# Kernel tuning notes

Measured on AMD Instinct MI355X. Metric: run time of the kernel, lower is better.

Reference implementation:

```python
import jax, jax.numpy as jnp
import numpy as np

CV_CHAN = 49  # displacement channels; radius = (CV_CHAN - 1) // 2 = 24


def conv1x1(x, W, b):
    # x: [B,C,H,Wd], W: [O,C], b: [O] -> [B,O,H,Wd]
    return jnp.einsum('oc,bchw->bohw', W, x) + b[None, :, None, None]


def corr_volume(f1, f2, radius, eps):
    """Shift-and-dot correlation along width. f1,f2: [B,C,H,W] -> [B,2r+1,H,W].
    Channel k corresponds to displacement d = k - radius; out-of-range positions are 0
    (handled by zero-padding, matching the torch zero-filled shifted tensors)."""
    f1n = f1 / (jnp.linalg.norm(f1, axis=1, keepdims=True) + eps)
    f2n = f2 / (jnp.linalg.norm(f2, axis=1, keepdims=True) + eps)
    Wd = f1.shape[3]
    pad = jnp.pad(f2n, ((0, 0), (0, 0), (0, 0), (radius, radius)))
    # shifted_k[x] = f2n[x - d] = pad[x + 2*radius - k]
    slices = [
        jnp.sum(f1n * jax.lax.dynamic_slice_in_dim(pad, 2 * radius - k, Wd, axis=3), axis=1)
        for k in range(2 * radius + 1)
    ]
    return jnp.stack(slices, axis=1)


def setup_inputs() -> dict:
    key = jax.random.key(0)
    ks = jax.random.split(key, 10)
    B, C, H, W = 4, 128, 128, 256
    F = 128  # fmap channels
    G = 96   # geo encoder output channels
    s = 0.05
    return {
        'feat_l1': jax.random.normal(ks[0], (B, C, H, W), jnp.float32),
        'feat_r1': jax.random.normal(ks[1], (B, C, H, W), jnp.float32),
        'cv0': jax.random.normal(ks[2], (B, CV_CHAN, H, W), jnp.float32),
        'cv1': jax.random.normal(ks[3], (B, CV_CHAN, H, W), jnp.float32),
        'cv2': jax.random.normal(ks[4], (B, CV_CHAN, H, W), jnp.float32),
        'W_f1': jax.random.normal(ks[5], (F, C), jnp.float32) * s,
        'b_f1': jnp.zeros((F,), jnp.float32),
        'W_f2': jax.random.normal(ks[6], (F, C), jnp.float32) * s,
        'b_f2': jnp.zeros((F,), jnp.float32),
        'W_geo': jax.random.normal(ks[7], (G, CV_CHAN), jnp.float32) * s,
        'b_geo': jnp.zeros((G,), jnp.float32),
        'W_sel': jax.random.normal(ks[8], (3, 3 * G), jnp.float32) * s,
        'b_sel': jnp.zeros((3,), jnp.float32),
    }


def reference(feat_l1, feat_r1, cv0, cv1, cv2,
              W_f1, b_f1, W_f2, b_f2, W_geo, b_geo, W_sel, b_sel):
    # init feature maps (init_fmap1 / init_fmap2 as 1x1 convs)
    fmap1 = conv1x1(feat_l1, W_f1, b_f1)
    fmap2 = conv1x1(feat_r1, W_f2, b_f2)
    radius = (CV_CHAN - 1) // 2
    init_corr = corr_volume(fmap1, fmap2, radius, 1e-8)  # [B, CV_CHAN, H, W]

    # geo_volume2 (1x1 conv CV_CHAN -> 96) applied to each geometric volume
    g0 = conv1x1(cv0, W_geo, b_geo)
    g1 = conv1x1(cv1, W_geo, b_geo)
    g2 = conv1x1(cv2, W_geo, b_geo)
    combined_g = jnp.concatenate([g0, g1, g2], axis=1)  # [B, 288, H, W]

    logits = conv1x1(combined_g, W_sel, b_sel)           # [B, 3, H, W]
    w = jax.nn.softmax(logits, axis=1)

    weighted = (w[:, 0:1] * cv0[:, :CV_CHAN]
                + w[:, 1:2] * cv1[:, :CV_CHAN]
                + w[:, 2:3] * cv2[:, :CV_CHAN])
    final = init_corr + weighted
    return (final, init_corr, w)
```

## Files before the change

kernel.cpp:

```cpp
#include <hip/hip_runtime.h>

#define HW 32768
#define WIDTH 256

typedef float f32x4 __attribute__((ext_vector_type(4)));
typedef short s16x8 __attribute__((ext_vector_type(8)));

__device__ __forceinline__ unsigned short f2bf(float f){
    unsigned int u = __float_as_uint(f);
    u += 0x7FFFu + ((u >> 16) & 1u);
    return (unsigned short)(u >> 16);
}
__device__ __forceinline__ unsigned int pk2(float a, float b){
    return (unsigned int)f2bf(a) | ((unsigned int)f2bf(b) << 16);
}

__global__ __launch_bounds__(256, 2) void k_fmap(
    const float* __restrict__ fl, const float* __restrict__ fr,
    const float* __restrict__ W1, const float* __restrict__ W2,
    const float* __restrict__ b1, const float* __restrict__ b2,
    unsigned short* __restrict__ f1N, unsigned short* __restrict__ f2N)
{
    const int z = blockIdx.z;
    const float* feat = z ? fr : fl;
    const float* Wm   = z ? W2 : W1;
    const float* bias = z ? b2 : b1;
    unsigned short* out = z ? f2N : f1N;

    const int b    = blockIdx.y;
    const int pxb  = blockIdx.x * 256;
    const int tid  = threadIdx.x;
    const int wv   = tid >> 6;
    const int lane = tid & 63;
    const int quad = lane >> 4;
    const int l15  = lane & 15;

    __shared__ unsigned short Xs[32][260];
    __shared__ unsigned short Ws[128][40];

    f32x4 acc[8][4];
    #pragma unroll
    for (int m = 0; m < 8; ++m)
        #pragma unroll
        for (int nt = 0; nt < 4; ++nt)
            acc[m][nt] = (f32x4){0.f,0.f,0.f,0.f};

    const float* featB = feat + (size_t)b * 128 * HW + pxb;

    for (int kk = 0; kk < 4; ++kk){
        const int kc0 = kk * 32;
        __syncthreads();
        #pragma unroll
        for (int i = 0; i < 8; ++i){
            int u   = tid + i * 256;
            int row = u >> 6;
            int cp  = (u & 63) << 2;
            f32x4 v = *(const f32x4*)(featB + (size_t)(kc0 + row) * HW + cp);
            uint2 pk; pk.x = pk2(v[0], v[1]); pk.y = pk2(v[2], v[3]);
            *(uint2*)&Xs[row][cp] = pk;
        }
        #pragma unroll
        for (int i = 0; i < 4; ++i){
            int u   = tid + i * 256;
            int row = u >> 3;
            int cp  = (u & 7) << 2;
            f32x4 v = *(const f32x4*)(Wm + row * 128 + kc0 + cp);
            uint2 pk; pk.x = pk2(v[0], v[1]); pk.y = pk2(v[2], v[3]);
            *(uint2*)&Ws[row][cp] = pk;
        }
        __syncthreads();

        s16x8 af[8];
        #pragma unroll
        for (int m = 0; m < 8; ++m)
            af[m] = *(const s16x8*)&Ws[m * 16 + l15][quad * 8];

        #pragma unroll
        for (int nt = 0; nt < 4; ++nt){
            const int px = wv * 64 + nt * 16 + l15;
            s16x8 bf;
            #pragma unroll
            for (int j = 0; j < 8; ++j)
                bf[j] = (short)Xs[quad * 8 + j][px];
            #pragma unroll
            for (int m = 0; m < 8; ++m)
                acc[m][nt] = __builtin_amdgcn_mfma_f32_16x16x32_bf16(af[m], bf, acc[m][nt], 0, 0, 0);
        }
    }

    #pragma unroll
    for (int nt = 0; nt < 4; ++nt){
        const int px = wv * 64 + nt * 16 + l15;
        #pragma unroll
        for (int m = 0; m < 8; ++m){
            f32x4 bv = *(const f32x4*)(bias + m * 16 + quad * 4);
            acc[m][nt] += bv;
        }
        float n2 = 0.f;
        #pragma unroll
        for (int m = 0; m < 8; ++m)
            #pragma unroll
            for (int r = 0; r < 4; ++r)
                n2 += acc[m][nt][r] * acc[m][nt][r];
        n2 += __shfl_xor(n2, 16, 64);
        n2 += __shfl_xor(n2, 32, 64);
        const float scale = 1.f / (sqrtf(n2) + 1e-8f);
        unsigned short* orow = out + ((size_t)b * HW + pxb + px) * 128;
        #pragma unroll
        for (int m = 0; m < 8; ++m){
            uint2 pk;
            pk.x = pk2(acc[m][nt][0] * scale, acc[m][nt][1] * scale);
            pk.y = pk2(acc[m][nt][2] * scale, acc[m][nt][3] * scale);
            *(uint2*)(orow + m * 16 + quad * 4) = pk;
        }
    }
}

__global__ __launch_bounds__(256, 4) void k_corr(
    const unsigned short* __restrict__ f1N,
    const unsigned short* __restrict__ f2N,
    float* __restrict__ ic)
{
    const int tid  = threadIdx.x;
    const int wv   = tid >> 6;
    const int lane = tid & 63;
    const int quad = lane >> 4;
    const int l15  = lane & 15;

    const int strip = blockIdx.x * 4 + wv;
    const int b   = strip >> 11;
    const int rem = strip & 2047;
    const int h   = rem >> 4;
    const int x0  = (rem & 15) << 4;

    const size_t rowbase = (size_t)b * HW + (size_t)h * WIDTH;

    const unsigned short* arow = f1N + (rowbase + x0 + l15) * 128;
    s16x8 af[4];
    #pragma unroll
    for (int kk = 0; kk < 4; ++kk)
        af[kk] = *(const s16x8*)(arow + kk * 32 + quad * 8);

    f32x4 acc[4];
    #pragma unroll
    for (int nt = 0; nt < 4; ++nt) acc[nt] = (f32x4){0.f,0.f,0.f,0.f};

    #pragma unroll
    for (int nt = 0; nt < 4; ++nt){
        const int s = x0 + nt * 16 + l15 - 24;
        const bool valid = (s >= 0) && (s < WIDTH);
        const unsigned short* brow = f2N + (rowbase + s) * 128;
        #pragma unroll
        for (int kk = 0; kk < 4; ++kk){
            s16x8 bf = (s16x8){0,0,0,0,0,0,0,0};
            if (valid) bf = *(const s16x8*)(brow + kk * 32 + quad * 8);
            acc[nt] = __builtin_amdgcn_mfma_f32_16x16x32_bf16(af[kk], bf, acc[nt], 0, 0, 0);
        }
    }

    __shared__ float G[4][16][68];
    #pragma unroll
    for (int nt = 0; nt < 4; ++nt)
        #pragma unroll
        for (int r = 0; r < 4; ++r)
            G[wv][quad * 4 + r][nt * 16 + l15] = acc[nt][r];
    __syncthreads();

    float* obase = ic + (size_t)b * 49 * HW + (size_t)h * WIDTH + x0;
    #pragma unroll
    for (int i = 0; i < 13; ++i){
        int dd = quad + i * 4;
        if (dd < 49){
            float v = G[wv][l15][l15 + 48 - dd];
            obase[(size_t)dd * HW + l15] = v;
        }
    }
}

__global__ void k_prep(const float* __restrict__ Wsel, const float* __restrict__ bsel,
                       const float* __restrict__ Wgeo, const float* __restrict__ bgeo,
                       float* __restrict__ M, float* __restrict__ c0)
{
    int u = threadIdx.x;
    if (u < 441){
        int s = u / 147; int r = u % 147; int i = r / 49; int k = r % 49;
        float acc = 0.f;
        for (int o = 0; o < 96; ++o)
            acc += Wsel[s * 288 + i * 96 + o] * Wgeo[o * 49 + k];
        M[u] = acc;
    } else if (u < 444){
        int s = u - 441;
        float acc = bsel[s];
        for (int i = 0; i < 3; ++i)
            for (int o = 0; o < 96; ++o)
                acc += Wsel[s * 288 + i * 96 + o] * bgeo[o];
        c0[s] = acc;
    }
}

__global__ __launch_bounds__(256, 4) void k_sel(
    const float* __restrict__ cv0, const float* __restrict__ cv1, const float* __restrict__ cv2,
    const float* __restrict__ M, const float* __restrict__ c0,
    const float* __restrict__ ic,
    float* __restrict__ finalO, float* __restrict__ wO)
{
    __shared__ float Ms[441];
    __shared__ float c0s[3];
    const int tid = threadIdx.x;
    for (int i = tid; i < 441; i += 256) Ms[i] = M[i];
    if (tid < 3) c0s[tid] = c0[tid];
    __syncthreads();

    const int gid = blockIdx.x * 256 + tid;
    const int b = gid >> 15;
    const int p = gid & 32767;
    const size_t base = (size_t)b * 49 * HW + p;

    float lg0 = c0s[0], lg1 = c0s[1], lg2 = c0s[2];
    for (int k = 0; k < 49; ++k){
        size_t o = base + (size_t)k * HW;
        float v0 = cv0[o], v1 = cv1[o], v2 = cv2[o];
        lg0 += Ms[k]       * v0 + Ms[49  + k] * v1 + Ms[98  + k] * v2;
        lg1 += Ms[147 + k] * v0 + Ms[196 + k] * v1 + Ms[245 + k] * v2;
        lg2 += Ms[294 + k] * v0 + Ms[343 + k] * v1 + Ms[392 + k] * v2;
    }
    float mx = fmaxf(lg0, fmaxf(lg1, lg2));
    float e0 = expf(lg0 - mx), e1 = expf(lg1 - mx), e2 = expf(lg2 - mx);
    float inv = 1.f / (e0 + e1 + e2);
    float w0 = e0 * inv, w1 = e1 * inv, w2 = e2 * inv;

    const size_t wbase = (size_t)b * 3 * HW + p;
    wO[wbase]          = w0;
    wO[wbase + HW]     = w1;
    wO[wbase + 2 * HW] = w2;

    for (int k = 0; k < 49; ++k){
        size_t o = base + (size_t)k * HW;
        finalO[o] = ic[o] + w0 * cv0[o] + w1 * cv1[o] + w2 * cv2[o];
    }
}

extern "C" void kernel_launch(void* const* d_in, const int* in_sizes, int n_in,
                              void* d_out, int out_size, void* d_ws, size_t ws_size,
                              hipStream_t stream)
{
    const float* feat_l1 = (const float*)d_in[0];
    const float* feat_r1 = (const float*)d_in[1];
    const float* cv0     = (const float*)d_in[2];
    const float* cv1     = (const float*)d_in[3];
    const float* cv2     = (const float*)d_in[4];
    const float* W_f1    = (const float*)d_in[5];
    const float* b_f1    = (const float*)d_in[6];
    const float* W_f2    = (const float*)d_in[7];
    const float* b_f2    = (const float*)d_in[8];
    const float* W_geo   = (const float*)d_in[9];
    const float* b_geo   = (const float*)d_in[10];
    const float* W_sel   = (const float*)d_in[11];
    const float* b_sel   = (const float*)d_in[12];

    float* finalO = (float*)d_out;
    float* icO    = (float*)d_out + 6422528;
    float* wO     = (float*)d_out + 12845056;

    unsigned short* f1N = (unsigned short*)d_ws;
    unsigned short* f2N = (unsigned short*)((char*)d_ws + 33554432);
    float* Mbuf  = (float*)((char*)d_ws + 67108864);
    float* c0buf = Mbuf + 441;

    k_prep<<<1, 512, 0, stream>>>(W_sel, b_sel, W_geo, b_geo, Mbuf, c0buf);
    k_fmap<<<dim3(128, 4, 2), 256, 0, stream>>>(feat_l1, feat_r1, W_f1, W_f2, b_f1, b_f2, f1N, f2N);
    k_corr<<<2048, 256, 0, stream>>>(f1N, f2N, icO);
    k_sel<<<512, 256, 0, stream>>>(cv0, cv1, cv2, Mbuf, c0buf, icO, finalO, wO);
}
```

Baseline: 307.0 us.

## Load fmap operands directly from global, stage output through LDS, cache cv values in registers

The fmap GEMM now reads weights and features straight from global memory into bf16 MFMA fragments instead of staging them in shared memory. The normalized output is transposed through a shared tile so each thread writes contiguous 16-byte chunks. The selection kernel keeps all 147 cv values per pixel in registers, so the second pass no longer re-reads cv0/1/2, and its occupancy hint is lowered to fit that register use. The risks are strided, uncoalesced feature loads in the GEMM and register pressure or spills in k_sel.

```diff
diff --git a/kernel.cpp b/kernel.cpp
--- a/kernel.cpp
+++ b/kernel.cpp
@@ -35,9 +35,6 @@
     const int quad = lane >> 4;
     const int l15  = lane & 15;
 
-    __shared__ unsigned short Xs[32][260];
-    __shared__ unsigned short Ws[128][40];
-
     f32x4 acc[8][4];
     #pragma unroll
     for (int m = 0; m < 8; ++m)
@@ -47,50 +44,44 @@
 
     const float* featB = feat + (size_t)b * 128 * HW + pxb;
 
+    #pragma unroll
     for (int kk = 0; kk < 4; ++kk){
         const int kc0 = kk * 32;
-        __syncthreads();
-        #pragma unroll
-        for (int i = 0; i < 8; ++i){
-            int u   = tid + i * 256;
-            int row = u >> 6;
-            int cp  = (u & 63) << 2;
-            f32x4 v = *(const f32x4*)(featB + (size_t)(kc0 + row) * HW + cp);
-            uint2 pk; pk.x = pk2(v[0], v[1]); pk.y = pk2(v[2], v[3]);
-            *(uint2*)&Xs[row][cp] = pk;
-        }
-        #pragma unroll
-        for (int i = 0; i < 4; ++i){
-            int u   = tid + i * 256;
-            int row = u >> 3;
-            int cp  = (u & 7) << 2;
-            f32x4 v = *(const f32x4*)(Wm + row * 128 + kc0 + cp);
-            uint2 pk; pk.x = pk2(v[0], v[1]); pk.y = pk2(v[2], v[3]);
-            *(uint2*)&Ws[row][cp] = pk;
-        }
-        __syncthreads();
 
         s16x8 af[8];
         #pragma unroll
-        for (int m = 0; m < 8; ++m)
-            af[m] = *(const s16x8*)&Ws[m * 16 + l15][quad * 8];
+        for (int m = 0; m < 8; ++m){
+            const float* wp = Wm + (m * 16 + l15) * 128 + kc0 + quad * 8;
+            f32x4 w0 = *(const f32x4*)wp;
+            f32x4 w1 = *(const f32x4*)(wp + 4);
+            union { unsigned int u[4]; s16x8 v; } r;
+            r.u[0] = pk2(w0[0], w0[1]); r.u[1] = pk2(w0[2], w0[3]);
+            r.u[2] = pk2(w1[0], w1[1]); r.u[3] = pk2(w1[2], w1[3]);
+            af[m] = r.v;
+        }
 
         #pragma unroll
         for (int nt = 0; nt < 4; ++nt){
             const int px = wv * 64 + nt * 16 + l15;
-            s16x8 bf;
+            const float* bp = featB + (size_t)(kc0 + quad * 8) * HW + px;
+            float x[8];
             #pragma unroll
             for (int j = 0; j < 8; ++j)
-                bf[j] = (short)Xs[quad * 8 + j][px];
+                x[j] = bp[(size_t)j * HW];
+            union { unsigned int u[4]; s16x8 v; } r;
+            r.u[0] = pk2(x[0], x[1]); r.u[1] = pk2(x[2], x[3]);
+            r.u[2] = pk2(x[4], x[5]); r.u[3] = pk2(x[6], x[7]);
+            const s16x8 bf = r.v;
             #pragma unroll
             for (int m = 0; m < 8; ++m)
                 acc[m][nt] = __builtin_amdgcn_mfma_f32_16x16x32_bf16(af[m], bf, acc[m][nt], 0, 0, 0);
         }
     }
 
-    #pragma unroll
+    __shared__ unsigned short Ts[64][132];
+
     for (int nt = 0; nt < 4; ++nt){
-        const int px = wv * 64 + nt * 16 + l15;
+        __syncthreads();
         #pragma unroll
         for (int m = 0; m < 8; ++m){
             f32x4 bv = *(const f32x4*)(bias + m * 16 + quad * 4);
@@ -105,13 +96,29 @@
         n2 += __shfl_xor(n2, 16, 64);
         n2 += __shfl_xor(n2, 32, 64);
         const float scale = 1.f / (sqrtf(n2) + 1e-8f);
-        unsigned short* orow = out + ((size_t)b * HW + pxb + px) * 128;
+
+        unsigned short* trow = &Ts[wv * 16 + l15][0];
         #pragma unroll
         for (int m = 0; m < 8; ++m){
             uint2 pk;
             pk.x = pk2(acc[m][nt][0] * scale, acc[m][nt][1] * scale);
             pk.y = pk2(acc[m][nt][2] * scale, acc[m][nt][3] * scale);
-            *(uint2*)(orow + m * 16 + quad * 4) = pk;
+            *(uint2*)(trow + m * 16 + quad * 4) = pk;
+        }
+        __syncthreads();
+
+        const int s  = tid >> 2;
+        const int ch = tid & 3;
+        const int wvs = s >> 4, ls = s & 15;
+        const int gpx = pxb + wvs * 64 + nt * 16 + ls;
+        const unsigned short* src = &Ts[s][ch * 32];
+        unsigned short* dst = out + ((size_t)b * HW + gpx) * 128 + ch * 32;
+        #pragma unroll
+        for (int i = 0; i < 4; ++i){
+            union { struct { uint2 a, c; } p; s16x8 v; } m;
+            m.p.a = *(const uint2*)(src + i * 8);
+            m.p.c = *(const uint2*)(src + i * 8 + 4);
+            *(s16x8*)(dst + i * 8) = m.v;
         }
     }
 }
@@ -198,7 +205,7 @@
     }
 }
 
-__global__ __launch_bounds__(256, 4) void k_sel(
+__global__ __launch_bounds__(256, 2) void k_sel(
     const float* __restrict__ cv0, const float* __restrict__ cv1, const float* __restrict__ cv2,
     const float* __restrict__ M, const float* __restrict__ c0,
     const float* __restrict__ ic,
@@ -216,13 +223,19 @@
     const int p = gid & 32767;
     const size_t base = (size_t)b * 49 * HW + p;
 
-    float lg0 = c0s[0], lg1 = c0s[1], lg2 = c0s[2];
+    float a0[49], a1[49], a2[49];
+    #pragma unroll
     for (int k = 0; k < 49; ++k){
         size_t o = base + (size_t)k * HW;
-        float v0 = cv0[o], v1 = cv1[o], v2 = cv2[o];
-        lg0 += Ms[k]       * v0 + Ms[49  + k] * v1 + Ms[98  + k] * v2;
-        lg1 += Ms[147 + k] * v0 + Ms[196 + k] * v1 + Ms[245 + k] * v2;
-        lg2 += Ms[294 + k] * v0 + Ms[343 + k] * v1 + Ms[392 + k] * v2;
+        a0[k] = cv0[o]; a1[k] = cv1[o]; a2[k] = cv2[o];
+    }
+
+    float lg0 = c0s[0], lg1 = c0s[1], lg2 = c0s[2];
+    #pragma unroll
+    for (int k = 0; k < 49; ++k){
+        lg0 += Ms[k]       * a0[k] + Ms[49  + k] * a1[k] + Ms[98  + k] * a2[k];
+        lg1 += Ms[147 + k] * a0[k] + Ms[196 + k] * a1[k] + Ms[245 + k] * a2[k];
+        lg2 += Ms[294 + k] * a0[k] + Ms[343 + k] * a1[k] + Ms[392 + k] * a2[k];
     }
     float mx = fmaxf(lg0, fmaxf(lg1, lg2));
     float e0 = expf(lg0 - mx), e1 = expf(lg1 - mx), e2 = expf(lg2 - mx);
@@ -234,9 +247,10 @@
     wO[wbase + HW]     = w1;
     wO[wbase + 2 * HW] = w2;
 
+    #pragma unroll
     for (int k = 0; k < 49; ++k){
         size_t o = base + (size_t)k * HW;
-        finalO[o] = ic[o] + w0 * cv0[o] + w1 * cv1[o] + w2 * cv2[o];
+        finalO[o] = ic[o] + w0 * a0[k] + w1 * a1[k] + w2 * a2[k];
     }
 }
 
```

After: 301.7 us. About the same (-1.7%).
